# Performance work log

Hardware: AMD Instinct MI355X
Metric: run time of the kernel (lower is better)

The kernel has to match this reference:

```python
import jax, jax.numpy as jnp
import numpy as np

OUT = 8192   # out_features
IN = 8192    # in_features
GS = 64      # HQQ group_size (axis=0 grouping)
NG = OUT * IN // GS   # number of quantization groups = 1048576
B = 64       # tokens in the batch


def setup_inputs() -> dict:
    key = jax.random.key(0)
    k1, k2, k3, k4, k5 = jax.random.split(key, 5)
    x = jax.random.normal(k1, (B, IN), dtype=jnp.float32)
    # packed 4-bit weights: two 4-bit values per byte, packed along axis 0
    # (HQQ pack_4bit_u8: packed = (W[:GS//2] << 4) | W[GS//2:])
    W_q = jax.random.randint(k2, (GS // 2, NG), 0, 256, dtype=jnp.int32)
    scale = jax.random.uniform(k3, (1, NG), dtype=jnp.float32, minval=0.001, maxval=0.02)
    zero = jax.random.uniform(k4, (1, NG), dtype=jnp.float32, minval=0.0, maxval=15.0)
    bias = jax.random.normal(k5, (OUT,), dtype=jnp.float32) * 0.01
    return {"x": x, "W_q": W_q, "scale": scale, "zero": zero, "bias": bias}


def reference(x, W_q, scale, zero, bias):
    # Unpack 4-bit: high nibble holds rows [0, GS//2), low nibble rows [GS//2, GS)
    hi = (W_q >> 4).astype(jnp.float32)          # (GS//2, NG)
    lo = (W_q & 0xF).astype(jnp.float32)         # (GS//2, NG)
    Wu = jnp.concatenate([hi, lo], axis=0)       # (GS, NG)
    # HQQ group-wise dequant: W = (W_q - zero) * scale, then reshape to (out, in)
    W = ((Wu - zero) * scale).reshape(OUT, IN)
    # linear: y = x @ W^T + bias
    return x @ W.T + bias
```

## Files before the change

### kernel.cpp

```cpp
#include <hip/hip_runtime.h>
#include <stdint.h>

#define OUT_F 8192
#define IN_F  8192
#define NGRP  1048576
#define BATCH 64
#define KS    4
#define NSTEP ((IN_F / KS) / 128)

typedef float f32x4  __attribute__((ext_vector_type(4)));
typedef float f32x16 __attribute__((ext_vector_type(16)));
typedef _Float16 half8_t __attribute__((ext_vector_type(8)));

static __device__ __forceinline__ unsigned int pk_fma_f16(unsigned int a, unsigned int b, unsigned int c) {
  unsigned int d;
  asm("v_pk_fma_f16 %0, %1, %2, %3" : "=v"(d) : "v"(a), "v"(b), "v"(c));
  return d;
}
static __device__ __forceinline__ unsigned int pk16(float a, float b) {
  unsigned short ua = __builtin_bit_cast(unsigned short, (_Float16)a);
  unsigned short ub = __builtin_bit_cast(unsigned short, (_Float16)b);
  return (unsigned int)ua | ((unsigned int)ub << 16);
}

#define GLL16(g, l)                                                         \
  __builtin_amdgcn_global_load_lds(                                         \
      (const __attribute__((address_space(1))) void*)(g),                   \
      (__attribute__((address_space(3))) void*)(l), 16, 0, 0)

__global__ __launch_bounds__(256) void pre_kernel(const float* __restrict__ x, ushort* __restrict__ xh,
                                                  const float* __restrict__ scale, const float* __restrict__ zero,
                                                  uint32_t* __restrict__ szb) {
  const int b = blockIdx.x;
  if (b < 512) {
    const int i = b * 256 + threadIdx.x;
    float4 v = ((const float4*)x)[i];
    ushort4 o;
    o.x = __builtin_bit_cast(unsigned short, (_Float16)v.x);
    o.y = __builtin_bit_cast(unsigned short, (_Float16)v.y);
    o.z = __builtin_bit_cast(unsigned short, (_Float16)v.z);
    o.w = __builtin_bit_cast(unsigned short, (_Float16)v.w);
    ((ushort4*)xh)[i] = o;
  } else {
    const int i = (b - 512) * 256 + threadIdx.x;
    float4 s = ((const float4*)scale)[i];
    float4 z = ((const float4*)zero)[i];
    uint4 o;
    o.x = pk16(s.x, s.y);
    o.y = pk16(-(64.f + z.x) * s.x, -(64.f + z.y) * s.y);
    o.z = pk16(s.z, s.w);
    o.w = pk16(-(64.f + z.z) * s.z, -(64.f + z.w) * s.w);
    ((uint4*)szb)[i] = o;
  }
}

__global__ __launch_bounds__(256, 2) void hqq_gemm_kernel(
    const int* __restrict__ Wq, const uint32_t* __restrict__ szb,
    const ushort* __restrict__ xh, float* __restrict__ part)
{
  __shared__ ushort xlds[3][64 * 128];
  __shared__ ushort blds[2][64 * 128];

  const int t    = threadIdx.x;
  const int bid  = blockIdx.x;
  const int ks   = bid & 3;
  const int c    = bid >> 2;
  const int lane = t & 63;
  const int wid  = t >> 6;
  const int kbase = ks * (IN_F / KS);

  const int lr = t >> 5;
  const int i0 = (t & 31) * 4;
  const int* __restrict__ wq0 = Wq + (size_t)lr * NGRP + (size_t)c * IN_F + kbase + i0;
  const int* __restrict__ wq1 = wq0 + (size_t)8 * NGRP;
  const int* __restrict__ wq2 = wq0 + (size_t)16 * NGRP;
  const int* __restrict__ wq3 = wq0 + (size_t)24 * NGRP;
  const uint8_t* __restrict__ szp =
      (const uint8_t*)szb + ((size_t)c * IN_F + kbase + i0) * 4;
  const int wb0 = (i0 * 2) ^ ((lr & 7) << 4);

  const int mh   = wid & 1;
  const int nh   = wid >> 1;
  const int ln31 = lane & 31;
  const int koct = lane >> 5;
  const int arow = mh * 32 + ln31;
  const int brow = nh * 32 + ln31;

  f32x16 acc = {0.f, 0.f, 0.f, 0.f, 0.f, 0.f, 0.f, 0.f,
                0.f, 0.f, 0.f, 0.f, 0.f, 0.f, 0.f, 0.f};

  auto stage_x = [&](int bi, int s) {
    #pragma unroll
    for (int j = 0; j < 4; ++j) {
      const int m    = wid * 16 + j * 4 + (lane >> 4);
      const int scol = ((lane & 15) * 16) ^ ((m & 7) << 4);
      const ushort* g = xh + (size_t)m * IN_F + kbase + s * 128 + (scol >> 1);
      GLL16(g, &xlds[bi][(wid * 16 + j * 4) * 128]);
    }
  };

  auto ldregs = [&](int s, int4& w0, int4& w1, int4& w2, int4& w3, uint4& z4) {
    w0 = *(const int4*)(wq0 + (size_t)s * 128);
    w1 = *(const int4*)(wq1 + (size_t)s * 128);
    w2 = *(const int4*)(wq2 + (size_t)s * 128);
    w3 = *(const int4*)(wq3 + (size_t)s * 128);
    z4 = *(const uint4*)(szp + (size_t)s * 512);
  };

  auto stage_b = [&](int bi, const int4& w0, const int4& w1, const int4& w2, const int4& w3,
                     const uint4& z4) {
    uint8_t* bb = (uint8_t*)&blds[bi][0];
    auto dqrow = [&](const int4& wv, int r) {
      unsigned tt0 = ((unsigned)wv.y << 16) | (unsigned)wv.x;
      unsigned tt1 = ((unsigned)wv.w << 16) | (unsigned)wv.z;
      uint2 hh, ll;
      hh.x = pk_fma_f16((tt0 & 0x00F000F0u) | 0x54005400u, z4.x, z4.y);
      hh.y = pk_fma_f16((tt1 & 0x00F000F0u) | 0x54005400u, z4.z, z4.w);
      ll.x = pk_fma_f16(((tt0 << 4) & 0x00F000F0u) | 0x54005400u, z4.x, z4.y);
      ll.y = pk_fma_f16(((tt1 << 4) & 0x00F000F0u) | 0x54005400u, z4.z, z4.w);
      *(uint2*)(bb + r * 256 + wb0)        = hh;
      *(uint2*)(bb + (r + 32) * 256 + wb0) = ll;
    };
    dqrow(w0, lr);
    dqrow(w1, lr + 8);
    dqrow(w2, lr + 16);
    dqrow(w3, lr + 24);
  };

  {
    int4 a0, a1, a2, a3; uint4 z0;
    ldregs(0, a0, a1, a2, a3, z0);
    stage_b(0, a0, a1, a2, a3, z0);
  }
  stage_x(0, 0);
  stage_x(1, 1);
  int4 w0, w1, w2, w3; uint4 z4;
  ldregs(1, w0, w1, w2, w3, z4);

  int xr0 = 0, xr1 = 1, xr2 = 2;

  #pragma unroll 1
  for (int s = 0; s < NSTEP; ++s) {
    asm volatile("s_waitcnt lgkmcnt(0)" ::: "memory");
    __builtin_amdgcn_s_barrier();

    const bool more2 = (s + 2 < NSTEP);
    int4 n0, n1, n2, n3; uint4 nz;
    if (more2) {
      stage_x(xr2, s + 2);
      ldregs(s + 2, n0, n1, n2, n3, nz);
    }

    if (more2)               asm volatile("s_waitcnt vmcnt(18)" ::: "memory");
    else if (s + 1 < NSTEP)  asm volatile("s_waitcnt vmcnt(9)" ::: "memory");
    else                     asm volatile("s_waitcnt vmcnt(0)" ::: "memory");
    __builtin_amdgcn_sched_barrier(0);

    const uint8_t* xb   = (const uint8_t*)&xlds[xr0][0];
    const uint8_t* bbuf = (const uint8_t*)&blds[s & 1][0];
    #pragma unroll
    for (int kk = 0; kk < 8; ++kk) {
      const int colb = (kk * 16 + koct * 8) * 2;
      half8_t a = *(const half8_t*)(xb   + arow * 256 + (colb ^ ((arow & 7) << 4)));
      half8_t b = *(const half8_t*)(bbuf + brow * 256 + (colb ^ ((brow & 7) << 4)));
      acc = __builtin_amdgcn_mfma_f32_32x32x16_f16(a, b, acc, 0, 0, 0);
    }

    if (s + 1 < NSTEP) stage_b((s + 1) & 1, w0, w1, w2, w3, z4);
    if (more2) { w0 = n0; w1 = n1; w2 = n2; w3 = n3; z4 = nz; }

    const int tmp = xr0; xr0 = xr1; xr1 = xr2; xr2 = tmp;
  }

  const int o = ln31 * 128 + c + nh * 4096;
  const int mbase = mh * 32 + 4 * koct;
  float* bp = part + ((size_t)ks * OUT_F + o) * BATCH + mbase;
  #pragma unroll
  for (int q = 0; q < 4; ++q) {
    *(float4*)(bp + 8 * q) = (float4){acc[4 * q], acc[4 * q + 1], acc[4 * q + 2], acc[4 * q + 3]};
  }
}

__global__ __launch_bounds__(256) void reduce_kernel(const float* __restrict__ part,
                                                     const float* __restrict__ bias,
                                                     float* __restrict__ out)
{
  __shared__ float tile[32][65];
  const int ob = blockIdx.x;
  const int t  = threadIdx.x;
  {
    const int ol = t >> 3;
    const int mg = t & 7;
    const int o  = ob * 32 + ol;
    const size_t base = (size_t)o * BATCH + mg * 8;
    float s[8] = {0, 0, 0, 0, 0, 0, 0, 0};
    #pragma unroll
    for (int ks = 0; ks < KS; ++ks) {
      const float* p = part + (size_t)ks * OUT_F * BATCH + base;
      float4 a = *(const float4*)p;
      float4 b = *(const float4*)(p + 4);
      s[0] += a.x; s[1] += a.y; s[2] += a.z; s[3] += a.w;
      s[4] += b.x; s[5] += b.y; s[6] += b.z; s[7] += b.w;
    }
    const float bv = bias[o];
    #pragma unroll
    for (int j = 0; j < 8; ++j) tile[ol][mg * 8 + j] = s[j] + bv;
  }
  __syncthreads();
  {
    const int m  = t >> 2;
    const int og = (t & 3) * 8;
    float r[8];
    #pragma unroll
    for (int j = 0; j < 8; ++j) r[j] = tile[og + j][m];
    float* op = out + (size_t)m * OUT_F + ob * 32 + og;
    *(float4*)op       = (float4){r[0], r[1], r[2], r[3]};
    *(float4*)(op + 4) = (float4){r[4], r[5], r[6], r[7]};
  }
}

__global__ void hqq_fallback_kernel(const float* __restrict__ x, const int* __restrict__ Wq,
                                    const float* __restrict__ scale, const float* __restrict__ zero,
                                    const float* __restrict__ bias, float* __restrict__ out)
{
  int idx = blockIdx.x * blockDim.x + threadIdx.x;
  int b = idx >> 13;
  int o = idx & 8191;
  int g = o >> 7, cc = o & 127;
  int r = g & 31;
  bool hi = (g < 32);
  const int*   wrow = Wq    + (size_t)r  * NGRP + (size_t)cc * IN_F;
  const float* srow = scale + (size_t)cc * IN_F;
  const float* zrow = zero  + (size_t)cc * IN_F;
  const float* xrow = x     + (size_t)b  * IN_F;
  float acc = 0.f;
  for (int k = 0; k < IN_F; ++k) {
    int v = wrow[k];
    float nib = (float)(hi ? (v >> 4) : (v & 15));
    acc += xrow[k] * ((nib - zrow[k]) * srow[k]);
  }
  out[idx] = acc + bias[o];
}

extern "C" void kernel_launch(void* const* d_in, const int* in_sizes, int n_in,
                              void* d_out, int out_size, void* d_ws, size_t ws_size,
                              hipStream_t stream) {
  const float* x     = (const float*)d_in[0];
  const int*   Wq    = (const int*)d_in[1];
  const float* scale = (const float*)d_in[2];
  const float* zero  = (const float*)d_in[3];
  const float* bias  = (const float*)d_in[4];
  float* out = (float*)d_out;

  const size_t xh_bytes   = (size_t)BATCH * IN_F * sizeof(ushort);
  const size_t sz_bytes   = (size_t)NGRP * 4;
  const size_t part_bytes = (size_t)KS * BATCH * OUT_F * sizeof(float);

  if (ws_size >= xh_bytes + sz_bytes + part_bytes) {
    ushort*   xh   = (ushort*)d_ws;
    uint32_t* szb  = (uint32_t*)((char*)d_ws + xh_bytes);
    float*    part = (float*)((char*)d_ws + xh_bytes + sz_bytes);
    pre_kernel<<<1536, 256, 0, stream>>>(x, xh, scale, zero, szb);
    hqq_gemm_kernel<<<128 * KS, 256, 0, stream>>>(Wq, szb, xh, part);
    reduce_kernel<<<OUT_F / 32, 256, 0, stream>>>(part, bias, out);
  } else {
    hqq_fallback_kernel<<<(BATCH * OUT_F) / 256, 256, 0, stream>>>(x, Wq, scale, zero, bias, out);
  }
}
```

Before: 42.01 us.

## Double workgroup to 512 threads with intra-block K split and LDS reduction

The GEMM workgroup grows from 256 to 512 threads. The extra four waves split each 128-wide K step in half (kh), so every wave issues 4 MFMAs per step instead of 8, and each thread loads and dequantises half as many weight rows. After the main loop the two K-halves are combined through LDS, reusing the B buffer, before the partial sums are written out. This targets latency hiding and load parallelism per block. The cost is an extra barrier and LDS round trip at the end, plus fewer MFMAs per wave between barriers.

```diff
diff --git a/kernel.cpp b/kernel.cpp
--- a/kernel.cpp
+++ b/kernel.cpp
@@ -54,7 +54,7 @@
   }
 }
 
-__global__ __launch_bounds__(256, 2) void hqq_gemm_kernel(
+__global__ __launch_bounds__(512, 4) void hqq_gemm_kernel(
     const int* __restrict__ Wq, const uint32_t* __restrict__ szb,
     const ushort* __restrict__ xh, float* __restrict__ part)
 {
@@ -72,15 +72,14 @@
   const int lr = t >> 5;
   const int i0 = (t & 31) * 4;
   const int* __restrict__ wq0 = Wq + (size_t)lr * NGRP + (size_t)c * IN_F + kbase + i0;
-  const int* __restrict__ wq1 = wq0 + (size_t)8 * NGRP;
-  const int* __restrict__ wq2 = wq0 + (size_t)16 * NGRP;
-  const int* __restrict__ wq3 = wq0 + (size_t)24 * NGRP;
+  const int* __restrict__ wq1 = wq0 + (size_t)16 * NGRP;
   const uint8_t* __restrict__ szp =
       (const uint8_t*)szb + ((size_t)c * IN_F + kbase + i0) * 4;
   const int wb0 = (i0 * 2) ^ ((lr & 7) << 4);
 
-  const int mh   = wid & 1;
-  const int nh   = wid >> 1;
+  const int kh   = wid & 1;
+  const int mh   = (wid >> 1) & 1;
+  const int nh   = wid >> 2;
   const int ln31 = lane & 31;
   const int koct = lane >> 5;
   const int arow = mh * 32 + ln31;
@@ -91,24 +90,21 @@
 
   auto stage_x = [&](int bi, int s) {
     #pragma unroll
-    for (int j = 0; j < 4; ++j) {
-      const int m    = wid * 16 + j * 4 + (lane >> 4);
+    for (int j = 0; j < 2; ++j) {
+      const int m    = wid * 8 + j * 4 + (lane >> 4);
       const int scol = ((lane & 15) * 16) ^ ((m & 7) << 4);
       const ushort* g = xh + (size_t)m * IN_F + kbase + s * 128 + (scol >> 1);
-      GLL16(g, &xlds[bi][(wid * 16 + j * 4) * 128]);
+      GLL16(g, &xlds[bi][(wid * 8 + j * 4) * 128]);
     }
   };
 
-  auto ldregs = [&](int s, int4& w0, int4& w1, int4& w2, int4& w3, uint4& z4) {
+  auto ldregs = [&](int s, int4& w0, int4& w1, uint4& z4) {
     w0 = *(const int4*)(wq0 + (size_t)s * 128);
     w1 = *(const int4*)(wq1 + (size_t)s * 128);
-    w2 = *(const int4*)(wq2 + (size_t)s * 128);
-    w3 = *(const int4*)(wq3 + (size_t)s * 128);
     z4 = *(const uint4*)(szp + (size_t)s * 512);
   };
 
-  auto stage_b = [&](int bi, const int4& w0, const int4& w1, const int4& w2, const int4& w3,
-                     const uint4& z4) {
+  auto stage_b = [&](int bi, const int4& w0, const int4& w1, const uint4& z4) {
     uint8_t* bb = (uint8_t*)&blds[bi][0];
     auto dqrow = [&](const int4& wv, int r) {
       unsigned tt0 = ((unsigned)wv.y << 16) | (unsigned)wv.x;
@@ -122,20 +118,18 @@
       *(uint2*)(bb + (r + 32) * 256 + wb0) = ll;
     };
     dqrow(w0, lr);
-    dqrow(w1, lr + 8);
-    dqrow(w2, lr + 16);
-    dqrow(w3, lr + 24);
+    dqrow(w1, lr + 16);
   };
 
   {
-    int4 a0, a1, a2, a3; uint4 z0;
-    ldregs(0, a0, a1, a2, a3, z0);
-    stage_b(0, a0, a1, a2, a3, z0);
+    int4 a0, a1; uint4 z0;
+    ldregs(0, a0, a1, z0);
+    stage_b(0, a0, a1, z0);
   }
   stage_x(0, 0);
   stage_x(1, 1);
-  int4 w0, w1, w2, w3; uint4 z4;
-  ldregs(1, w0, w1, w2, w3, z4);
+  int4 w0, w1; uint4 z4;
+  ldregs(1, w0, w1, z4);
 
   int xr0 = 0, xr1 = 1, xr2 = 2;
 
@@ -145,39 +139,54 @@
     __builtin_amdgcn_s_barrier();
 
     const bool more2 = (s + 2 < NSTEP);
-    int4 n0, n1, n2, n3; uint4 nz;
+    int4 n0, n1; uint4 nz;
     if (more2) {
       stage_x(xr2, s + 2);
-      ldregs(s + 2, n0, n1, n2, n3, nz);
-    }
-
-    if (more2)               asm volatile("s_waitcnt vmcnt(18)" ::: "memory");
-    else if (s + 1 < NSTEP)  asm volatile("s_waitcnt vmcnt(9)" ::: "memory");
+      ldregs(s + 2, n0, n1, nz);
+    }
+
+    if (more2)               asm volatile("s_waitcnt vmcnt(10)" ::: "memory");
+    else if (s + 1 < NSTEP)  asm volatile("s_waitcnt vmcnt(5)" ::: "memory");
     else                     asm volatile("s_waitcnt vmcnt(0)" ::: "memory");
     __builtin_amdgcn_sched_barrier(0);
 
     const uint8_t* xb   = (const uint8_t*)&xlds[xr0][0];
     const uint8_t* bbuf = (const uint8_t*)&blds[s & 1][0];
     #pragma unroll
-    for (int kk = 0; kk < 8; ++kk) {
+    for (int j = 0; j < 4; ++j) {
+      const int kk   = kh * 4 + j;
       const int colb = (kk * 16 + koct * 8) * 2;
       half8_t a = *(const half8_t*)(xb   + arow * 256 + (colb ^ ((arow & 7) << 4)));
       half8_t b = *(const half8_t*)(bbuf + brow * 256 + (colb ^ ((brow & 7) << 4)));
       acc = __builtin_amdgcn_mfma_f32_32x32x16_f16(a, b, acc, 0, 0, 0);
     }
 
-    if (s + 1 < NSTEP) stage_b((s + 1) & 1, w0, w1, w2, w3, z4);
-    if (more2) { w0 = n0; w1 = n1; w2 = n2; w3 = n3; z4 = nz; }
+    if (s + 1 < NSTEP) stage_b((s + 1) & 1, w0, w1, z4);
+    if (more2) { w0 = n0; w1 = n1; z4 = nz; }
 
     const int tmp = xr0; xr0 = xr1; xr1 = xr2; xr2 = tmp;
   }
 
-  const int o = ln31 * 128 + c + nh * 4096;
-  const int mbase = mh * 32 + 4 * koct;
-  float* bp = part + ((size_t)ks * OUT_F + o) * BATCH + mbase;
-  #pragma unroll
-  for (int q = 0; q < 4; ++q) {
-    *(float4*)(bp + 8 * q) = (float4){acc[4 * q], acc[4 * q + 1], acc[4 * q + 2], acc[4 * q + 3]};
+  __syncthreads();
+  float* red = (float*)&blds[0][0];
+  {
+    float4* dst = (float4*)(red + ((size_t)(wid * 64 + lane)) * 16);
+    dst[0] = (float4){acc[0],  acc[1],  acc[2],  acc[3]};
+    dst[1] = (float4){acc[4],  acc[5],  acc[6],  acc[7]};
+    dst[2] = (float4){acc[8],  acc[9],  acc[10], acc[11]};
+    dst[3] = (float4){acc[12], acc[13], acc[14], acc[15]};
+  }
+  __syncthreads();
+  if (kh == 0) {
+    const float4* src = (const float4*)(red + ((size_t)((wid ^ 1) * 64 + lane)) * 16);
+    float4 p0 = src[0], p1 = src[1], p2 = src[2], p3 = src[3];
+    const int o = ln31 * 128 + c + nh * 4096;
+    const int mbase = mh * 32 + 4 * koct;
+    float* bp = part + ((size_t)ks * OUT_F + o) * BATCH + mbase;
+    *(float4*)(bp +  0) = (float4){acc[0]  + p0.x, acc[1]  + p0.y, acc[2]  + p0.z, acc[3]  + p0.w};
+    *(float4*)(bp +  8) = (float4){acc[4]  + p1.x, acc[5]  + p1.y, acc[6]  + p1.z, acc[7]  + p1.w};
+    *(float4*)(bp + 16) = (float4){acc[8]  + p2.x, acc[9]  + p2.y, acc[10] + p2.z, acc[11] + p2.w};
+    *(float4*)(bp + 24) = (float4){acc[12] + p3.x, acc[13] + p3.y, acc[14] + p3.z, acc[15] + p3.w};
   }
 }
 
@@ -261,7 +270,7 @@
     uint32_t* szb  = (uint32_t*)((char*)d_ws + xh_bytes);
     float*    part = (float*)((char*)d_ws + xh_bytes + sz_bytes);
     pre_kernel<<<1536, 256, 0, stream>>>(x, xh, scale, zero, szb);
-    hqq_gemm_kernel<<<128 * KS, 256, 0, stream>>>(Wq, szb, xh, part);
+    hqq_gemm_kernel<<<128 * KS, 512, 0, stream>>>(Wq, szb, xh, part);
     reduce_kernel<<<OUT_F / 32, 256, 0, stream>>>(part, bias, out);
   } else {
     hqq_fallback_kernel<<<(BATCH * OUT_F) / 256, 256, 0, stream>>>(x, Wq, scale, zero, bias, out);
```

After: 40.73 us. 1.03x faster.
